# Kernel optimization log

Measured on AMD Instinct MI355X. Metric: run time of the kernel, lower is better.

Reference implementation:

```python
import jax, jax.numpy as jnp
import numpy as np

N_INPUTS = 4
ACTIVE_IDX = 0
HIDDEN = 2048
EPS = 1e-6
ROUTER_INPUT_SCALE = float(HIDDEN ** (-1.0))


def _rms_norm(x, w, eps=EPS):
    var = jnp.mean(jnp.square(x), axis=-1, keepdims=True)
    return x * jax.lax.rsqrt(var + eps) * w


def _modalities(x, w_norm, W_router):
    # tanh(router(norm(x) * hidden_size**-1)) -> [B, S, n]
    r = _rms_norm(x, w_norm) * ROUTER_INPUT_SCALE
    return jnp.tanh(r @ W_router.T)


def setup_inputs() -> dict:
    key = jax.random.key(0)
    k0, k1, k2, k3, k4 = jax.random.split(key, 5)
    B, S = 2, 4096
    return {
        "hidden_states": jax.random.normal(k0, (N_INPUTS, B, S, HIDDEN), jnp.float32),
        "activated": jax.random.normal(k1, (B, S, HIDDEN), jnp.float32),
        "w_norm": jnp.ones((HIDDEN,), jnp.float32),
        "W_router": jax.random.normal(k2, (N_INPUTS, HIDDEN), jnp.float32) * 0.02,
        "W_pred": jax.random.normal(k3, (N_INPUTS * N_INPUTS, N_INPUTS), jnp.float32) * 0.02,
        "W_corr": jax.random.normal(k4, (N_INPUTS, N_INPUTS), jnp.float32) * 0.02,
    }


def reference(hidden_states, activated, w_norm, W_router, W_pred, W_corr):
    n = N_INPUTS
    # ---- predict ----
    active = hidden_states[ACTIVE_IDX]                      # [B,S,H]
    mods = _modalities(active, w_norm, W_router)            # [B,S,n]
    coefs = (mods @ W_pred.T)                               # [B,S,n*n]
    coefs = coefs.reshape(*coefs.shape[:-1], n, n)          # [B,S,n,n]
    coefs = jnp.swapaxes(coefs, -1, -2)                     # transpose last two dims
    stacked = jnp.moveaxis(hidden_states, 0, -1)            # [B,S,H,n]
    preds = jnp.einsum('bshk,bskj->bshj', stacked, coefs) + stacked
    predictions = jnp.moveaxis(preds, -1, 0)                # [n,B,S,H]
    # ---- correct ----
    mods_c = _modalities(activated, w_norm, W_router)       # [B,S,n]
    innovation = activated - predictions[ACTIVE_IDX]        # [B,S,H]
    ccoefs = mods_c @ W_corr.T + 1.0                        # [B,S,n]
    corrected = predictions + innovation[None] * jnp.moveaxis(ccoefs, -1, 0)[..., None]
    return corrected                                        # [n,B,S,H]
```

## Files before the change

### kernel.cpp

```cpp
#include <hip/hip_runtime.h>


constexpr int H = 2048;
constexpr float EPS = 1e-6f;

__global__ __launch_bounds__(256) void altup_fused(
    const float* __restrict__ hs,
    const float* __restrict__ act,
    const float* __restrict__ w_norm,
    const float* __restrict__ W_router,
    const float* __restrict__ W_pred,
    const float* __restrict__ W_corr,
    float* __restrict__ out,
    long long T)
{
    const long long t = blockIdx.x;
    const int tid = threadIdx.x;
    const long long row = t * (long long)H;
    const long long plane = T * (long long)H;

    __shared__ float s_x0[H];
    __shared__ float s_xc[H];
    __shared__ float s_red[4][10];

    float p[10];
#pragma unroll
    for (int i = 0; i < 10; ++i) p[i] = 0.f;

#pragma unroll
    for (int c = 0; c < 2; ++c) {
        const int h = c * 1024 + tid * 4;
        const float4 xa4 = *reinterpret_cast<const float4*>(hs + row + h);
        const float4 xc4 = *reinterpret_cast<const float4*>(act + row + h);
        const float4 wn4 = *reinterpret_cast<const float4*>(w_norm + h);
        *reinterpret_cast<float4*>(s_x0 + h) = xa4;
        *reinterpret_cast<float4*>(s_xc + h) = xc4;
        const float* a = &xa4.x;
        const float* cc = &xc4.x;
        const float* w = &wn4.x;
#pragma unroll
        for (int e = 0; e < 4; ++e) {
            p[0] += a[e] * a[e];
            p[5] += cc[e] * cc[e];
        }
#pragma unroll
        for (int i = 0; i < 4; ++i) {
            const float4 wr4 = *reinterpret_cast<const float4*>(W_router + i * H + h);
            const float* r = &wr4.x;
#pragma unroll
            for (int e = 0; e < 4; ++e) {
                p[1 + i] += a[e] * w[e] * r[e];
                p[6 + i] += cc[e] * w[e] * r[e];
            }
        }
    }

#pragma unroll
    for (int m = 1; m < 64; m <<= 1) {
#pragma unroll
        for (int i = 0; i < 10; ++i) p[i] += __shfl_xor(p[i], m, 64);
    }
    const int wave = tid >> 6;
    const int lane = tid & 63;
    if (lane == 0) {
#pragma unroll
        for (int i = 0; i < 10; ++i) s_red[wave][i] = p[i];
    }
    __syncthreads();

    float tot[10];
#pragma unroll
    for (int i = 0; i < 10; ++i)
        tot[i] = s_red[0][i] + s_red[1][i] + s_red[2][i] + s_red[3][i];

    const float ris = 1.0f / (float)H;
    const float inv_a = rsqrtf(tot[0] * ris + EPS) * ris;
    const float inv_c = rsqrtf(tot[5] * ris + EPS) * ris;
    float mods[4], modsc[4];
#pragma unroll
    for (int i = 0; i < 4; ++i) {
        mods[i]  = tanhf(tot[1 + i] * inv_a);
        modsc[i] = tanhf(tot[6 + i] * inv_c);
    }
    float coefT[4][4];
#pragma unroll
    for (int j = 0; j < 4; ++j)
#pragma unroll
        for (int k = 0; k < 4; ++k) {
            float s = 0.f;
#pragma unroll
            for (int m = 0; m < 4; ++m) s += mods[m] * W_pred[(j * 4 + k) * 4 + m];
            coefT[k][j] = s;
        }
    float ccoef[4];
#pragma unroll
    for (int j = 0; j < 4; ++j) {
        float s = 1.0f;
#pragma unroll
        for (int m = 0; m < 4; ++m) s += modsc[m] * W_corr[j * 4 + m];
        ccoef[j] = s;
    }

#pragma unroll
    for (int c = 0; c < 2; ++c) {
        const int h = c * 1024 + tid * 4;
        float4 xk4[4];
        xk4[0] = *reinterpret_cast<const float4*>(s_x0 + h);
        xk4[1] = *reinterpret_cast<const float4*>(hs + plane + row + h);
        xk4[2] = *reinterpret_cast<const float4*>(hs + 2 * plane + row + h);
        xk4[3] = *reinterpret_cast<const float4*>(hs + 3 * plane + row + h);
        const float4 xc4 = *reinterpret_cast<const float4*>(s_xc + h);
        float4 o4[4];
#pragma unroll
        for (int e = 0; e < 4; ++e) {
            float xk[4];
#pragma unroll
            for (int k = 0; k < 4; ++k) xk[k] = (&xk4[k].x)[e];
            const float xce = (&xc4.x)[e];
            float pred[4];
#pragma unroll
            for (int j = 0; j < 4; ++j) {
                float s = xk[j];
#pragma unroll
                for (int k = 0; k < 4; ++k) s += xk[k] * coefT[k][j];
                pred[j] = s;
            }
            const float innov = xce - pred[0];
#pragma unroll
            for (int j = 0; j < 4; ++j)
                (&o4[j].x)[e] = pred[j] + innov * ccoef[j];
        }
#pragma unroll
        for (int j = 0; j < 4; ++j)
            *reinterpret_cast<float4*>(out + j * plane + row + h) = o4[j];
    }
}

extern "C" void kernel_launch(void* const* d_in, const int* in_sizes, int n_in,
                              void* d_out, int out_size, void* d_ws, size_t ws_size,
                              hipStream_t stream) {
    const float* hs       = (const float*)d_in[0];
    const float* act      = (const float*)d_in[1];
    const float* w_norm   = (const float*)d_in[2];
    const float* W_router = (const float*)d_in[3];
    const float* W_pred   = (const float*)d_in[4];
    const float* W_corr   = (const float*)d_in[5];
    float* out = (float*)d_out;
    const long long T = (long long)in_sizes[0] / (4LL * H);
    altup_fused<<<dim3((unsigned)T), dim3(256), 0, stream>>>(
        hs, act, w_norm, W_router, W_pred, W_corr, out, T);
}
```

Measured before the change: 128.5 us.

## Use 512-thread blocks, keep rows in registers and issue all loads upfront

The block grows from 256 to 512 threads so each thread handles one float4 per row instead of two. All five input streams (four hidden planes plus activated) are loaded into registers at the start, before the reduction, and the shared-memory staging of x0 and xc is removed. This aims to put more memory traffic in flight early and hide the latency of the plane 1-3 loads behind the reduction. In exchange, register pressure per thread rises and the cross-wave reduction now covers 8 waves.

```diff
diff --git a/kernel.cpp b/kernel.cpp
--- a/kernel.cpp
+++ b/kernel.cpp
@@ -4,7 +4,7 @@
 constexpr int H = 2048;
 constexpr float EPS = 1e-6f;
 
-__global__ __launch_bounds__(256) void altup_fused(
+__global__ __launch_bounds__(512) void altup_fused(
     const float* __restrict__ hs,
     const float* __restrict__ act,
     const float* __restrict__ w_norm,
@@ -18,40 +18,38 @@
     const int tid = threadIdx.x;
     const long long row = t * (long long)H;
     const long long plane = T * (long long)H;
+    const int h = tid * 4;
 
-    __shared__ float s_x0[H];
-    __shared__ float s_xc[H];
-    __shared__ float s_red[4][10];
+    __shared__ float s_red[8][10];
+
+    const float4 x0 = *reinterpret_cast<const float4*>(hs + row + h);
+    const float4 x1 = *reinterpret_cast<const float4*>(hs + plane + row + h);
+    const float4 x2 = *reinterpret_cast<const float4*>(hs + 2 * plane + row + h);
+    const float4 x3 = *reinterpret_cast<const float4*>(hs + 3 * plane + row + h);
+    const float4 xc = *reinterpret_cast<const float4*>(act + row + h);
+    const float4 wn = *reinterpret_cast<const float4*>(w_norm + h);
 
     float p[10];
+    {
+        const float* a = &x0.x;
+        const float* c = &xc.x;
+        const float* w = &wn.x;
+        float s0 = 0.f, s5 = 0.f;
 #pragma unroll
-    for (int i = 0; i < 10; ++i) p[i] = 0.f;
-
-#pragma unroll
-    for (int c = 0; c < 2; ++c) {
-        const int h = c * 1024 + tid * 4;
-        const float4 xa4 = *reinterpret_cast<const float4*>(hs + row + h);
-        const float4 xc4 = *reinterpret_cast<const float4*>(act + row + h);
-        const float4 wn4 = *reinterpret_cast<const float4*>(w_norm + h);
-        *reinterpret_cast<float4*>(s_x0 + h) = xa4;
-        *reinterpret_cast<float4*>(s_xc + h) = xc4;
-        const float* a = &xa4.x;
-        const float* cc = &xc4.x;
-        const float* w = &wn4.x;
-#pragma unroll
-        for (int e = 0; e < 4; ++e) {
-            p[0] += a[e] * a[e];
-            p[5] += cc[e] * cc[e];
-        }
+        for (int e = 0; e < 4; ++e) { s0 += a[e] * a[e]; s5 += c[e] * c[e]; }
+        p[0] = s0; p[5] = s5;
 #pragma unroll
         for (int i = 0; i < 4; ++i) {
             const float4 wr4 = *reinterpret_cast<const float4*>(W_router + i * H + h);
             const float* r = &wr4.x;
+            float da = 0.f, dc = 0.f;
 #pragma unroll
             for (int e = 0; e < 4; ++e) {
-                p[1 + i] += a[e] * w[e] * r[e];
-                p[6 + i] += cc[e] * w[e] * r[e];
+                const float wre = w[e] * r[e];
+                da += a[e] * wre;
+                dc += c[e] * wre;
             }
+            p[1 + i] = da; p[6 + i] = dc;
         }
     }
 
@@ -61,8 +59,7 @@
         for (int i = 0; i < 10; ++i) p[i] += __shfl_xor(p[i], m, 64);
     }
     const int wave = tid >> 6;
-    const int lane = tid & 63;
-    if (lane == 0) {
+    if ((tid & 63) == 0) {
 #pragma unroll
         for (int i = 0; i < 10; ++i) s_red[wave][i] = p[i];
     }
@@ -70,8 +67,12 @@
 
     float tot[10];
 #pragma unroll
-    for (int i = 0; i < 10; ++i)
-        tot[i] = s_red[0][i] + s_red[1][i] + s_red[2][i] + s_red[3][i];
+    for (int i = 0; i < 10; ++i) {
+        float s = 0.f;
+#pragma unroll
+        for (int wv = 0; wv < 8; ++wv) s += s_red[wv][i];
+        tot[i] = s;
+    }
 
     const float ris = 1.0f / (float)H;
     const float inv_a = rsqrtf(tot[0] * ris + EPS) * ris;
@@ -101,39 +102,31 @@
         ccoef[j] = s;
     }
 
+    const float* xk0 = &x0.x;
+    const float* xk1 = &x1.x;
+    const float* xk2 = &x2.x;
+    const float* xk3 = &x3.x;
+    const float* xce = &xc.x;
+    float4 o4[4];
 #pragma unroll
-    for (int c = 0; c < 2; ++c) {
-        const int h = c * 1024 + tid * 4;
-        float4 xk4[4];
-        xk4[0] = *reinterpret_cast<const float4*>(s_x0 + h);
-        xk4[1] = *reinterpret_cast<const float4*>(hs + plane + row + h);
-        xk4[2] = *reinterpret_cast<const float4*>(hs + 2 * plane + row + h);
-        xk4[3] = *reinterpret_cast<const float4*>(hs + 3 * plane + row + h);
-        const float4 xc4 = *reinterpret_cast<const float4*>(s_xc + h);
-        float4 o4[4];
+    for (int e = 0; e < 4; ++e) {
+        const float xk[4] = { xk0[e], xk1[e], xk2[e], xk3[e] };
+        float pred[4];
 #pragma unroll
-        for (int e = 0; e < 4; ++e) {
-            float xk[4];
+        for (int j = 0; j < 4; ++j) {
+            float s = xk[j];
 #pragma unroll
-            for (int k = 0; k < 4; ++k) xk[k] = (&xk4[k].x)[e];
-            const float xce = (&xc4.x)[e];
-            float pred[4];
-#pragma unroll
-            for (int j = 0; j < 4; ++j) {
-                float s = xk[j];
-#pragma unroll
-                for (int k = 0; k < 4; ++k) s += xk[k] * coefT[k][j];
-                pred[j] = s;
-            }
-            const float innov = xce - pred[0];
-#pragma unroll
-            for (int j = 0; j < 4; ++j)
-                (&o4[j].x)[e] = pred[j] + innov * ccoef[j];
+            for (int k = 0; k < 4; ++k) s += xk[k] * coefT[k][j];
+            pred[j] = s;
         }
+        const float innov = xce[e] - pred[0];
 #pragma unroll
         for (int j = 0; j < 4; ++j)
-            *reinterpret_cast<float4*>(out + j * plane + row + h) = o4[j];
+            (&o4[j].x)[e] = pred[j] + innov * ccoef[j];
     }
+#pragma unroll
+    for (int j = 0; j < 4; ++j)
+        *reinterpret_cast<float4*>(out + j * plane + row + h) = o4[j];
 }
 
 extern "C" void kernel_launch(void* const* d_in, const int* in_sizes, int n_in,
@@ -147,6 +140,6 @@
     const float* W_corr   = (const float*)d_in[5];
     float* out = (float*)d_out;
     const long long T = (long long)in_sizes[0] / (4LL * H);
-    altup_fused<<<dim3((unsigned)T), dim3(256), 0, stream>>>(
+    altup_fused<<<dim3((unsigned)T), dim3(512), 0, stream>>>(
         hs, act, w_norm, W_router, W_pred, W_corr, out, T);
 }
```

New measurement: 121.4 us. 5.6% less time.

## Preload all token planes into registers up front and drop shared staging

Applied to the files above, without the earlier changes.

The kernel now uses 128 threads per token and loads all five input rows (active, activated, and the other three hidden planes) into registers at the start, rather than staging two rows through shared memory and loading the other planes after the reduction. Issuing every global load before the reduction is meant to raise memory-level parallelism and hide the latency of the later loads behind the norm and router computation. In exchange each thread holds about 80 floats of live data, which raises register pressure and may cut occupancy. Output is written plane by plane, and pred[0] is recomputed for each output plane.

```diff
diff --git a/kernel.cpp b/kernel.cpp
--- a/kernel.cpp
+++ b/kernel.cpp
@@ -2,9 +2,12 @@
 
 
 constexpr int H = 2048;
+constexpr int NC = 4;
 constexpr float EPS = 1e-6f;
 
-__global__ __launch_bounds__(256) void altup_fused(
+typedef float f32x4 __attribute__((ext_vector_type(4)));
+
+__global__ __launch_bounds__(128) void altup_tok(
     const float* __restrict__ hs,
     const float* __restrict__ act,
     const float* __restrict__ w_norm,
@@ -14,44 +17,53 @@
     float* __restrict__ out,
     long long T)
 {
+    const int tid = threadIdx.x;
     const long long t = blockIdx.x;
-    const int tid = threadIdx.x;
     const long long row = t * (long long)H;
     const long long plane = T * (long long)H;
 
-    __shared__ float s_x0[H];
-    __shared__ float s_xc[H];
-    __shared__ float s_red[4][10];
+    __shared__ float s_red[2][10];
+
+    f32x4 x0[NC], xc[NC], x1[NC], x2[NC], x3[NC];
+#pragma unroll
+    for (int c = 0; c < NC; ++c)
+        x0[c] = *reinterpret_cast<const f32x4*>(hs + row + c * 512 + tid * 4);
+#pragma unroll
+    for (int c = 0; c < NC; ++c)
+        xc[c] = *reinterpret_cast<const f32x4*>(act + row + c * 512 + tid * 4);
+#pragma unroll
+    for (int c = 0; c < NC; ++c)
+        x1[c] = *reinterpret_cast<const f32x4*>(hs + plane + row + c * 512 + tid * 4);
+#pragma unroll
+    for (int c = 0; c < NC; ++c)
+        x2[c] = *reinterpret_cast<const f32x4*>(hs + 2 * plane + row + c * 512 + tid * 4);
+#pragma unroll
+    for (int c = 0; c < NC; ++c)
+        x3[c] = *reinterpret_cast<const f32x4*>(hs + 3 * plane + row + c * 512 + tid * 4);
 
     float p[10];
 #pragma unroll
     for (int i = 0; i < 10; ++i) p[i] = 0.f;
-
 #pragma unroll
-    for (int c = 0; c < 2; ++c) {
-        const int h = c * 1024 + tid * 4;
-        const float4 xa4 = *reinterpret_cast<const float4*>(hs + row + h);
-        const float4 xc4 = *reinterpret_cast<const float4*>(act + row + h);
-        const float4 wn4 = *reinterpret_cast<const float4*>(w_norm + h);
-        *reinterpret_cast<float4*>(s_x0 + h) = xa4;
-        *reinterpret_cast<float4*>(s_xc + h) = xc4;
-        const float* a = &xa4.x;
-        const float* cc = &xc4.x;
-        const float* w = &wn4.x;
+    for (int c = 0; c < NC; ++c) {
+        const int off = c * 512 + tid * 4;
+        const f32x4 wn = *reinterpret_cast<const f32x4*>(w_norm + off);
 #pragma unroll
         for (int e = 0; e < 4; ++e) {
-            p[0] += a[e] * a[e];
-            p[5] += cc[e] * cc[e];
+            p[0] += x0[c][e] * x0[c][e];
+            p[5] += xc[c][e] * xc[c][e];
         }
 #pragma unroll
         for (int i = 0; i < 4; ++i) {
-            const float4 wr4 = *reinterpret_cast<const float4*>(W_router + i * H + h);
-            const float* r = &wr4.x;
+            const f32x4 wr = *reinterpret_cast<const f32x4*>(W_router + i * H + off);
+            float da = 0.f, dc = 0.f;
 #pragma unroll
             for (int e = 0; e < 4; ++e) {
-                p[1 + i] += a[e] * w[e] * r[e];
-                p[6 + i] += cc[e] * w[e] * r[e];
+                const float wre = wn[e] * wr[e];
+                da += x0[c][e] * wre;
+                dc += xc[c][e] * wre;
             }
+            p[1 + i] += da; p[6 + i] += dc;
         }
     }
 
@@ -60,18 +72,15 @@
 #pragma unroll
         for (int i = 0; i < 10; ++i) p[i] += __shfl_xor(p[i], m, 64);
     }
-    const int wave = tid >> 6;
-    const int lane = tid & 63;
-    if (lane == 0) {
+    const int wv = tid >> 6;
+    if ((tid & 63) == 0) {
 #pragma unroll
-        for (int i = 0; i < 10; ++i) s_red[wave][i] = p[i];
+        for (int i = 0; i < 10; ++i) s_red[wv][i] = p[i];
     }
     __syncthreads();
-
     float tot[10];
 #pragma unroll
-    for (int i = 0; i < 10; ++i)
-        tot[i] = s_red[0][i] + s_red[1][i] + s_red[2][i] + s_red[3][i];
+    for (int i = 0; i < 10; ++i) tot[i] = s_red[0][i] + s_red[1][i];
 
     const float ris = 1.0f / (float)H;
     const float inv_a = rsqrtf(tot[0] * ris + EPS) * ris;
@@ -102,37 +111,23 @@
     }
 
 #pragma unroll
-    for (int c = 0; c < 2; ++c) {
-        const int h = c * 1024 + tid * 4;
-        float4 xk4[4];
-        xk4[0] = *reinterpret_cast<const float4*>(s_x0 + h);
-        xk4[1] = *reinterpret_cast<const float4*>(hs + plane + row + h);
-        xk4[2] = *reinterpret_cast<const float4*>(hs + 2 * plane + row + h);
-        xk4[3] = *reinterpret_cast<const float4*>(hs + 3 * plane + row + h);
-        const float4 xc4 = *reinterpret_cast<const float4*>(s_xc + h);
-        float4 o4[4];
+    for (int j = 0; j < 4; ++j) {
 #pragma unroll
-        for (int e = 0; e < 4; ++e) {
-            float xk[4];
+        for (int c = 0; c < NC; ++c) {
+            f32x4 o;
 #pragma unroll
-            for (int k = 0; k < 4; ++k) xk[k] = (&xk4[k].x)[e];
-            const float xce = (&xc4.x)[e];
-            float pred[4];
+            for (int e = 0; e < 4; ++e) {
+                const float xk[4] = { x0[c][e], x1[c][e], x2[c][e], x3[c][e] };
+                float pj = xk[j];
 #pragma unroll
-            for (int j = 0; j < 4; ++j) {
-                float s = xk[j];
+                for (int k = 0; k < 4; ++k) pj += xk[k] * coefT[k][j];
+                float p0 = xk[0];
 #pragma unroll
-                for (int k = 0; k < 4; ++k) s += xk[k] * coefT[k][j];
-                pred[j] = s;
+                for (int k = 0; k < 4; ++k) p0 += xk[k] * coefT[k][0];
+                o[e] = pj + (xc[c][e] - p0) * ccoef[j];
             }
-            const float innov = xce - pred[0];
-#pragma unroll
-            for (int j = 0; j < 4; ++j)
-                (&o4[j].x)[e] = pred[j] + innov * ccoef[j];
+            *reinterpret_cast<f32x4*>(out + j * plane + row + c * 512 + tid * 4) = o;
         }
-#pragma unroll
-        for (int j = 0; j < 4; ++j)
-            *reinterpret_cast<float4*>(out + j * plane + row + h) = o4[j];
     }
 }
 
@@ -147,6 +142,7 @@
     const float* W_corr   = (const float*)d_in[5];
     float* out = (float*)d_out;
     const long long T = (long long)in_sizes[0] / (4LL * H);
-    altup_fused<<<dim3((unsigned)T), dim3(256), 0, stream>>>(
+
+    altup_tok<<<dim3((unsigned)T), dim3(128), 0, stream>>>(
         hs, act, w_norm, W_router, W_pred, W_corr, out, T);
 }
```

Measured after the change: 117.1 us (median of 2 runs). -8.9%, faster.
